# Kernel tuning notes

Measured on AMD Instinct MI355X. Metric: run time of the kernel, lower is better.

The kernel has to match this reference:

```python
import jax, jax.numpy as jnp
import numpy as np

B, T, C = 4, 2048, 1024
N_HEAD = 16
HEAD_DIM = C // N_HEAD


def setup_inputs() -> dict:
    key = jax.random.key(0)
    kx, kk, kq, kv, kp = jax.random.split(key, 5)
    s = 1.0 / np.sqrt(C)
    return {
        "x": jax.random.normal(kx, (B, T, C), dtype=jnp.float32),
        "Wk": jax.random.normal(kk, (C, C), dtype=jnp.float32) * s,
        "Wq": jax.random.normal(kq, (C, C), dtype=jnp.float32) * s,
        "Wv": jax.random.normal(kv, (C, C), dtype=jnp.float32) * s,
        "Wp": jax.random.normal(kp, (C, C), dtype=jnp.float32) * s,
    }


def reference(x, Wk, Wq, Wv, Wp):
    b, t, c = x.shape
    # torch nn.Linear(y = x @ W.T); split heads -> [B, H, T, D]
    def heads(w):
        return jnp.einsum("btc,ec->bte", x, w).reshape(b, t, N_HEAD, HEAD_DIM).transpose(0, 2, 1, 3)
    k = heads(Wk)
    q = heads(Wq)
    v = heads(Wv)
    scale = 1.0 / np.sqrt(HEAD_DIM).astype(np.float32)
    att = jnp.einsum("bhqd,bhkd->bhqk", q, k) * scale  # [B,H,T,T]
    causal = jnp.tril(jnp.ones((t, t), dtype=bool))
    att = jnp.where(causal[None, None], att, -jnp.inf)
    att = jax.nn.softmax(att, axis=-1)
    y = jnp.einsum("bhqk,bhkd->bhqd", att, v)  # [B,H,T,D]
    y = y.transpose(0, 2, 1, 3).reshape(b, t, c)
    return jnp.einsum("btc,ec->bte", y, Wp)
```

## Files before the change

### kernel.cpp

```cpp
#include <hip/hip_runtime.h>

typedef __bf16 bf16x8 __attribute__((ext_vector_type(8)));
typedef float f32x4 __attribute__((ext_vector_type(4)));
typedef float f32x16 __attribute__((ext_vector_type(16)));
typedef unsigned short u16x8 __attribute__((ext_vector_type(8)));
typedef unsigned short u16x4 __attribute__((ext_vector_type(4)));
typedef unsigned u32x4 __attribute__((ext_vector_type(4)));

#define BB 4
#define TT 2048
#define CC 1024
#define HH 16
#define DD 64

__device__ __forceinline__ unsigned short f2bf(float f){
  unsigned u = __builtin_bit_cast(unsigned, f);
  u += 0x7FFFu + ((u >> 16) & 1u);
  return (unsigned short)(u >> 16);
}
__device__ __forceinline__ bf16x8 as_bf(u16x8 v){ return __builtin_bit_cast(bf16x8, v); }
__device__ __forceinline__ unsigned cvt_pk(float lo, float hi){
  unsigned r; asm("v_cvt_pk_bf16_f32 %0, %1, %2" : "=v"(r) : "v"(lo), "v"(hi)); return r;
}
__device__ __forceinline__ void pl32swap(unsigned &a, unsigned &b){
  asm("v_permlane32_swap_b32 %0, %1" : "+v"(a), "+v"(b));
}
__device__ __forceinline__ float ex2(float x){
#if __has_builtin(__builtin_amdgcn_exp2f)
  return __builtin_amdgcn_exp2f(x);
#else
  return __expf(x * 0.6931471805599453f);
#endif
}

__global__ __launch_bounds__(256) void cvt_all(const float* __restrict__ x,
                                               const float* __restrict__ Wk,
                                               const float* __restrict__ Wq,
                                               const float* __restrict__ Wv,
                                               const float* __restrict__ Wp,
                                               unsigned short* __restrict__ xb,
                                               unsigned short* __restrict__ wb){
  const int i = blockIdx.x * 256 + threadIdx.x;
  constexpr int EX = (BB*TT*CC)/4;
  const float* src; unsigned short* dst; int off;
  if (i < EX){ src = x; dst = xb; off = i; }
  else {
    const int j = i - EX;
    const int wsel = j >> 18;
    off = j & 262143;
    src = (wsel==0) ? Wk : (wsel==1) ? Wq : (wsel==2) ? Wv : Wp;
    dst = wb + ((size_t)wsel << 20);
  }
  const float4 f = ((const float4*)src)[off];
  u16x4 o; o.x = f2bf(f.x); o.y = f2bf(f.y); o.z = f2bf(f.z); o.w = f2bf(f.w);
  ((u16x4*)dst)[off] = o;
}

template<int NX, bool QKV>
__global__ __launch_bounds__(256) void gemm128(const unsigned short* __restrict__ A,
                                               const unsigned short* __restrict__ Bm,
                                               void* __restrict__ o0, void* __restrict__ o1,
                                               void* __restrict__ o2){
  constexpr int K = 1024;
  constexpr int NWG = NX * 64;
  __shared__ __align__(16) unsigned short As[128*64];
  __shared__ __align__(16) unsigned short Bs[128*64];
  const int tid = threadIdx.x;
  const int flat = blockIdx.y * NX + blockIdx.x;
  const int swz = (flat & 7) * (NWG / 8) + (flat >> 3);
  const int n0 = (swz % NX) * 128;
  const int m0 = (swz / NX) * 128;
  const int w = tid >> 6, lane = tid & 63, l15 = lane & 15, g = lane >> 4;
  const int wm = (w >> 1) * 64, wn = (w & 1) * 64;
  const int tsel = QKV ? (n0 >> 10) : 0;

  f32x4 acc[4][4] = {};

  for (int k0 = 0; k0 < K; k0 += 64){
    #pragma unroll
    for (int i = 0; i < 4; ++i){
      const int p = i*256 + tid;
      const int r = p >> 3, c = p & 7;
      const int gc = c ^ (r & 7);
      __builtin_amdgcn_global_load_lds(
        (const __attribute__((address_space(1))) void*)(A + (size_t)(m0 + r)*K + k0 + gc*8),
        (__attribute__((address_space(3))) void*)(As + p*8), 16, 0, 0);
    }
    #pragma unroll
    for (int i = 0; i < 4; ++i){
      const int p = i*256 + tid;
      const int r = p >> 3, c = p & 7;
      const int gc = c ^ (r & 7);
      __builtin_amdgcn_global_load_lds(
        (const __attribute__((address_space(1))) void*)(Bm + (size_t)(n0 + r)*K + k0 + gc*8),
        (__attribute__((address_space(3))) void*)(Bs + p*8), 16, 0, 0);
    }
    __syncthreads();

    bf16x8 af[2][4], bfr[2][4];
    #pragma unroll
    for (int ks = 0; ks < 2; ++ks){
      #pragma unroll
      for (int m = 0; m < 4; ++m){
        const int R = wm + m*16 + l15;
        const int c = (ks*4 + g) ^ (R & 7);
        af[ks][m] = as_bf(*(const u16x8*)(As + R*64 + c*8));
      }
      #pragma unroll
      for (int n = 0; n < 4; ++n){
        const int R = wn + n*16 + l15;
        const int c = (ks*4 + g) ^ (R & 7);
        bfr[ks][n] = as_bf(*(const u16x8*)(Bs + R*64 + c*8));
      }
    }
    #pragma unroll
    for (int ks = 0; ks < 2; ++ks)
      #pragma unroll
      for (int m = 0; m < 4; ++m)
        #pragma unroll
        for (int n = 0; n < 4; ++n)
          acc[m][n] = __builtin_amdgcn_mfma_f32_16x16x32_bf16(af[ks][m], bfr[ks][n], acc[m][n], 0, 0, 0);
    __syncthreads();
  }

  if (QKV && tsel == 2){
    const int bq = m0 >> 11;
    const int t0 = m0 & 2047;
    unsigned short* vt = (unsigned short*)o2;
    #pragma unroll
    for (int n = 0; n < 4; ++n){
      const int cg = (n0 & 1023) + wn + n*16 + l15;
      const int h = cg >> 6, d = cg & 63;
      unsigned short* base = vt + ((size_t)(bq*HH + h)*DD + d)*TT;
      #pragma unroll
      for (int m = 0; m < 4; ++m){
        const int t = t0 + wm + m*16 + g*4;
        const int kt = t >> 6;
        const int cch = ((t >> 3) & 7) ^ (d & 7);
        u16x4 pv;
        pv.x = f2bf(acc[m][n][0]); pv.y = f2bf(acc[m][n][1]);
        pv.z = f2bf(acc[m][n][2]); pv.w = f2bf(acc[m][n][3]);
        *(u16x4*)(base + (size_t)kt*64 + cch*8 + (t & 7)) = pv;
      }
    }
    return;
  }

  const float sc = (QKV && tsel == 1) ? 0.18033688011112042f : 1.0f;
  unsigned short* outb = nullptr;
  if (QKV) outb = (unsigned short*)(tsel == 0 ? o0 : o1);

  #pragma unroll
  for (int m = 0; m < 4; ++m)
    #pragma unroll
    for (int n = 0; n < 4; ++n)
      #pragma unroll
      for (int r = 0; r < 4; ++r){
        const int row = m0 + wm + m*16 + g*4 + r;
        const int col = n0 + wn + n*16 + l15;
        const float v = acc[m][n][r];
        if (QKV) outb[(size_t)row*1024 + (col & 1023)] = f2bf(v * sc);
        else     ((float*)o0)[(size_t)row*1024 + col] = v;
      }
}

__global__ __launch_bounds__(512, 4) void attn2(const unsigned short* __restrict__ Q,
                                                const unsigned short* __restrict__ Km,
                                                const unsigned short* __restrict__ Vt,
                                                unsigned short* __restrict__ Y){
  __shared__ __align__(16) unsigned short Ks[3][64*64];
  __shared__ __align__(16) unsigned short Vs[3][64*64];
  const int bh = blockIdx.x, b = bh >> 4, h = bh & 15;
  const int yq = blockIdx.y;
  const int qt = (yq < 4) ? (7 - yq) : (yq - 4);
  const int tid = threadIdx.x;
  const int w = tid >> 6, lane = tid & 63, l31 = lane & 31, hi = lane >> 5;
  const int q0 = qt * 256;
  const int wq0 = q0 + w * 32;
  const int wqmax = wq0 + 31;
  const int nkt = 4 * qt + 4;
  const int qg = wq0 + l31;

  const unsigned short* Ksrc = Km + (size_t)b*TT*CC + h*DD;
  const unsigned short* Vsrc = Vt + (size_t)bh*DD*TT;

  auto stage = [&](int buf, int kt){
    const int r = tid >> 3, c = tid & 7;
    const int gc = c ^ (r & 7);
    __builtin_amdgcn_global_load_lds(
      (const __attribute__((address_space(1))) void*)(Ksrc + (size_t)(kt*64 + r)*CC + gc*8),
      (__attribute__((address_space(3))) void*)(&Ks[buf][tid*8]), 16, 0, 0);
    __builtin_amdgcn_global_load_lds(
      (const __attribute__((address_space(1))) void*)(Vsrc + (size_t)r*TT + (size_t)kt*64 + c*8),
      (__attribute__((address_space(3))) void*)(&Vs[buf][tid*8]), 16, 0, 0);
  };

  stage(0, 0);

  const unsigned short* qrow = Q + ((size_t)b*TT + wq0 + l31)*CC + h*DD;
  bf16x8 qf[4];
  #pragma unroll
  for (int ds = 0; ds < 4; ++ds)
    qf[ds] = as_bf(*(const u16x8*)(qrow + 16*ds + 8*hi));

  int koff[4];
  #pragma unroll
  for (int ds = 0; ds < 4; ++ds)
    koff[ds] = l31*64 + (((2*ds + hi) ^ (l31 & 7)) * 8);

  float m_ = -1e30f, l_ = 0.f;
  f32x16 y0 = {}, y1 = {};

  int cb = 0;
  for (int t = 0; t < nkt; ++t){
    const int nx = (cb == 2) ? 0 : cb + 1;
    if (t + 1 < nkt){
      stage(nx, t + 1);
      asm volatile("s_waitcnt vmcnt(2)" ::: "memory");
    } else {
      asm volatile("s_waitcnt vmcnt(0)" ::: "memory");
    }
    __builtin_amdgcn_s_barrier();

    if (t*64 <= wqmax){
      const unsigned short* Kp = &Ks[cb][0];
      const unsigned short* Vp = &Vs[cb][0];

      f32x16 s0 = {}, s1 = {};
      __builtin_amdgcn_s_setprio(1);
      #pragma unroll
      for (int ds = 0; ds < 4; ++ds){
        bf16x8 kf0 = as_bf(*(const u16x8*)(Kp + koff[ds]));
        s0 = __builtin_amdgcn_mfma_f32_32x32x16_bf16(kf0, qf[ds], s0, 0, 0, 0);
        bf16x8 kf1 = as_bf(*(const u16x8*)(Kp + koff[ds] + 2048));
        s1 = __builtin_amdgcn_mfma_f32_32x32x16_bf16(kf1, qf[ds], s1, 0, 0, 0);
      }
      __builtin_amdgcn_s_setprio(0);

      if (t*64 + 63 > wq0){
        const int kb0 = t*64;
        #pragma unroll
        for (int r = 0; r < 16; ++r){
          const int kr = (r & 3) + 8*(r >> 2) + 4*hi;
          if (kb0 + kr      > qg) s0[r] = -1e30f;
          if (kb0 + 32 + kr > qg) s1[r] = -1e30f;
        }
      }

      float tm[8];
      #pragma unroll
      for (int r = 0; r < 8; ++r) tm[r] = fmaxf(fmaxf(s0[r], s0[r+8]), fmaxf(s1[r], s1[r+8]));
      #pragma unroll
      for (int r = 0; r < 4; ++r) tm[r] = fmaxf(tm[r], tm[r+4]);
      float pmax = fmaxf(fmaxf(tm[0], tm[2]), fmaxf(tm[1], tm[3]));
      pmax = fmaxf(pmax, __shfl_xor(pmax, 32));

      if (!__all(pmax <= m_ + 8.f)){
        const float mnew = fmaxf(m_, pmax);
        const float alpha = ex2(m_ - mnew);
        l_ *= alpha;
        #pragma unroll
        for (int r = 0; r < 16; ++r){
          const float ar = __shfl(alpha, (r & 3) + 8*(r >> 2) + 4*hi);
          y0[r] *= ar; y1[r] *= ar;
        }
        m_ = mnew;
      }

      #pragma unroll
      for (int r = 0; r < 16; ++r) s0[r] = ex2(s0[r] - m_);
      #pragma unroll
      for (int r = 0; r < 16; ++r) s1[r] = ex2(s1[r] - m_);
      float ts[8];
      #pragma unroll
      for (int r = 0; r < 8; ++r) ts[r] = (s0[r] + s0[r+8]) + (s1[r] + s1[r+8]);
      #pragma unroll
      for (int r = 0; r < 4; ++r) ts[r] += ts[r+4];
      float rs = (ts[0] + ts[2]) + (ts[1] + ts[3]);
      rs += __shfl_xor(rs, 32);
      l_ += rs;

      __builtin_amdgcn_s_setprio(1);
      #pragma unroll
      for (int m = 0; m < 4; ++m){
        const f32x16 c = (m < 2) ? s0 : s1;
        const int bx = (m & 1) * 8;
        unsigned A0 = cvt_pk(c[bx+0], c[bx+1]);
        unsigned B0 = cvt_pk(c[bx+4], c[bx+5]);
        pl32swap(A0, B0);
        unsigned A1 = cvt_pk(c[bx+2], c[bx+3]);
        unsigned B1 = cvt_pk(c[bx+6], c[bx+7]);
        pl32swap(A1, B1);
        u32x4 pw; pw.x = A0; pw.y = A1; pw.z = B0; pw.w = B1;
        const bf16x8 pa = __builtin_bit_cast(bf16x8, pw);
        bf16x8 vf0 = as_bf(*(const u16x8*)(Vp + koff[m]));
        y0 = __builtin_amdgcn_mfma_f32_32x32x16_bf16(pa, vf0, y0, 0, 0, 0);
        bf16x8 vf1 = as_bf(*(const u16x8*)(Vp + koff[m] + 2048));
        y1 = __builtin_amdgcn_mfma_f32_32x32x16_bf16(pa, vf1, y1, 0, 0, 0);
      }
      __builtin_amdgcn_s_setprio(0);
    }
    cb = nx;
  }

  const float linv = 1.f / l_;
  #pragma unroll
  for (int r = 0; r < 16; ++r){
    const int qlr = (r & 3) + 8*(r >> 2) + 4*hi;
    const float lr = __shfl(linv, qlr);
    unsigned short* yp = Y + ((size_t)b*TT + wq0 + qlr)*CC + h*DD + l31;
    yp[0]  = f2bf(y0[r] * lr);
    yp[32] = f2bf(y1[r] * lr);
  }
}

extern "C" void kernel_launch(void* const* d_in, const int* in_sizes, int n_in,
                              void* d_out, int out_size, void* d_ws, size_t ws_size,
                              hipStream_t stream){
  const float* x  = (const float*)d_in[0];
  const float* Wk = (const float*)d_in[1];
  const float* Wq = (const float*)d_in[2];
  const float* Wv = (const float*)d_in[3];
  const float* Wp = (const float*)d_in[4];

  const size_t E  = (size_t)BB*TT*CC;
  const size_t Wn = (size_t)CC*CC;
  unsigned short* ws  = (unsigned short*)d_ws;
  unsigned short* xb  = ws;
  unsigned short* wkb = xb  + E;
  unsigned short* wqb = wkb + Wn;
  unsigned short* wvb = wqb + Wn;
  unsigned short* wpb = wvb + Wn;
  unsigned short* qb  = wpb + Wn;
  unsigned short* kb  = qb  + E;
  unsigned short* vt  = kb  + E;

  cvt_all<<<12288, 256, 0, stream>>>(x, Wk, Wq, Wv, Wp, xb, wkb);

  gemm128<24, true><<<dim3(24, 64), 256, 0, stream>>>(xb, wkb, kb, qb, vt);

  unsigned short* yb = xb;
  attn2<<<dim3(BB*HH, TT/256), 512, 0, stream>>>(qb, kb, vt, yb);

  gemm128<8, false><<<dim3(8, 64), 256, 0, stream>>>(yb, wpb, (float*)d_out, nullptr, nullptr);
}
```

Baseline: 159.4 us.

## Use 256x256 double-buffered QKV GEMM with async LDS prefetch

Replaces the 128x128 single-buffered QKV projection GEMM with a 256x256-tile, 512-thread kernel. It uses 128KB of dynamic LDS for two stages, so the next K-tile's global-to-LDS loads are in flight while the current tile runs on MFMA, and it raises MFMA priority around the inner loop. The larger tile is meant to improve operand reuse and hide global latency. In exchange the grid shrinks to 384 workgroups with one per CU, which risks poor tail balance on a 256-CU part and higher register pressure from the 8x4 accumulator array.

```diff
diff --git a/kernel.cpp b/kernel.cpp
--- a/kernel.cpp
+++ b/kernel.cpp
@@ -56,11 +56,132 @@
   ((u16x4*)dst)[off] = o;
 }
 
-template<int NX, bool QKV>
+template<int NX>
+__global__ __launch_bounds__(512) void gemm256q(const unsigned short* __restrict__ A,
+                                                const unsigned short* __restrict__ Bm,
+                                                void* __restrict__ o0, void* __restrict__ o1,
+                                                void* __restrict__ o2){
+  constexpr int K = 1024;
+  constexpr int NKT = 16;
+  constexpr int NWG = NX * 32;
+  extern __shared__ unsigned short lds[];
+  const int tid = threadIdx.x;
+  const int flat = blockIdx.y * NX + blockIdx.x;
+  const int swz = (flat & 7) * (NWG / 8) + (flat >> 3);
+  const int n0 = (swz % NX) * 256;
+  const int m0 = (swz / NX) * 256;
+  const int w = tid >> 6, lane = tid & 63, l15 = lane & 15, g = lane >> 4;
+  const int wm = (w >> 2) * 128;
+  const int wn = (w & 3) * 64;
+  const int tsel = n0 >> 10;
+
+  auto stage = [&](int s, int kt){
+    unsigned short* Asl = lds + s*32768;
+    unsigned short* Bsl = Asl + 16384;
+    const int k0 = kt * 64;
+    #pragma unroll
+    for (int i = 0; i < 4; ++i){
+      const int p = i*512 + tid;
+      const int r = p >> 3, c = p & 7;
+      const int gc = c ^ (r & 7);
+      __builtin_amdgcn_global_load_lds(
+        (const __attribute__((address_space(1))) void*)(A + (size_t)(m0 + r)*K + k0 + gc*8),
+        (__attribute__((address_space(3))) void*)(Asl + p*8), 16, 0, 0);
+    }
+    #pragma unroll
+    for (int i = 0; i < 4; ++i){
+      const int p = i*512 + tid;
+      const int r = p >> 3, c = p & 7;
+      const int gc = c ^ (r & 7);
+      __builtin_amdgcn_global_load_lds(
+        (const __attribute__((address_space(1))) void*)(Bm + (size_t)(n0 + r)*K + k0 + gc*8),
+        (__attribute__((address_space(3))) void*)(Bsl + p*8), 16, 0, 0);
+    }
+  };
+
+  f32x4 acc[8][4] = {};
+  stage(0, 0);
+
+  for (int t = 0; t < NKT; ++t){
+    const int s = t & 1;
+    if (t + 1 < NKT){
+      stage(s ^ 1, t + 1);
+      asm volatile("s_waitcnt vmcnt(8)" ::: "memory");
+    } else {
+      asm volatile("s_waitcnt vmcnt(0)" ::: "memory");
+    }
+    __builtin_amdgcn_s_barrier();
+
+    const unsigned short* Asl = lds + s*32768;
+    const unsigned short* Bsl = Asl + 16384;
+
+    #pragma unroll
+    for (int ks = 0; ks < 2; ++ks){
+      bf16x8 b4[4];
+      #pragma unroll
+      for (int n = 0; n < 4; ++n){
+        const int R = wn + n*16 + l15;
+        const int c = (ks*4 + g) ^ (R & 7);
+        b4[n] = as_bf(*(const u16x8*)(Bsl + R*64 + c*8));
+      }
+      __builtin_amdgcn_s_setprio(1);
+      #pragma unroll
+      for (int m = 0; m < 8; ++m){
+        const int R = wm + m*16 + l15;
+        const int c = (ks*4 + g) ^ (R & 7);
+        bf16x8 a = as_bf(*(const u16x8*)(Asl + R*64 + c*8));
+        #pragma unroll
+        for (int n = 0; n < 4; ++n)
+          acc[m][n] = __builtin_amdgcn_mfma_f32_16x16x32_bf16(a, b4[n], acc[m][n], 0, 0, 0);
+      }
+      __builtin_amdgcn_s_setprio(0);
+    }
+
+    asm volatile("s_waitcnt lgkmcnt(0)" ::: "memory");
+    __builtin_amdgcn_s_barrier();
+  }
+
+  if (tsel == 2){
+    const int bq = m0 >> 11;
+    const int t0 = m0 & 2047;
+    unsigned short* vt = (unsigned short*)o2;
+    #pragma unroll
+    for (int n = 0; n < 4; ++n){
+      const int cg = (n0 & 1023) + wn + n*16 + l15;
+      const int h = cg >> 6, d = cg & 63;
+      unsigned short* base = vt + ((size_t)(bq*HH + h)*DD + d)*TT;
+      #pragma unroll
+      for (int m = 0; m < 8; ++m){
+        const int t = t0 + wm + m*16 + g*4;
+        const int kt = t >> 6;
+        const int cch = ((t >> 3) & 7) ^ (d & 7);
+        u16x4 pv;
+        pv.x = f2bf(acc[m][n][0]); pv.y = f2bf(acc[m][n][1]);
+        pv.z = f2bf(acc[m][n][2]); pv.w = f2bf(acc[m][n][3]);
+        *(u16x4*)(base + (size_t)kt*64 + cch*8 + (t & 7)) = pv;
+      }
+    }
+    return;
+  }
+
+  const float sc = (tsel == 1) ? 0.18033688011112042f : 1.0f;
+  unsigned short* outb = (unsigned short*)(tsel == 0 ? o0 : o1);
+  #pragma unroll
+  for (int m = 0; m < 8; ++m)
+    #pragma unroll
+    for (int n = 0; n < 4; ++n)
+      #pragma unroll
+      for (int r = 0; r < 4; ++r){
+        const int row = m0 + wm + m*16 + g*4 + r;
+        const int col = (n0 & 1023) + wn + n*16 + l15;
+        outb[(size_t)row*1024 + col] = f2bf(acc[m][n][r] * sc);
+      }
+}
+
+template<int NX>
 __global__ __launch_bounds__(256) void gemm128(const unsigned short* __restrict__ A,
                                                const unsigned short* __restrict__ Bm,
-                                               void* __restrict__ o0, void* __restrict__ o1,
-                                               void* __restrict__ o2){
+                                               float* __restrict__ o0){
   constexpr int K = 1024;
   constexpr int NWG = NX * 64;
   __shared__ __align__(16) unsigned short As[128*64];
@@ -72,7 +193,6 @@
   const int m0 = (swz / NX) * 128;
   const int w = tid >> 6, lane = tid & 63, l15 = lane & 15, g = lane >> 4;
   const int wm = (w >> 1) * 64, wn = (w & 1) * 64;
-  const int tsel = QKV ? (n0 >> 10) : 0;
 
   f32x4 acc[4][4] = {};
 
@@ -123,33 +243,6 @@
     __syncthreads();
   }
 
-  if (QKV && tsel == 2){
-    const int bq = m0 >> 11;
-    const int t0 = m0 & 2047;
-    unsigned short* vt = (unsigned short*)o2;
-    #pragma unroll
-    for (int n = 0; n < 4; ++n){
-      const int cg = (n0 & 1023) + wn + n*16 + l15;
-      const int h = cg >> 6, d = cg & 63;
-      unsigned short* base = vt + ((size_t)(bq*HH + h)*DD + d)*TT;
-      #pragma unroll
-      for (int m = 0; m < 4; ++m){
-        const int t = t0 + wm + m*16 + g*4;
-        const int kt = t >> 6;
-        const int cch = ((t >> 3) & 7) ^ (d & 7);
-        u16x4 pv;
-        pv.x = f2bf(acc[m][n][0]); pv.y = f2bf(acc[m][n][1]);
-        pv.z = f2bf(acc[m][n][2]); pv.w = f2bf(acc[m][n][3]);
-        *(u16x4*)(base + (size_t)kt*64 + cch*8 + (t & 7)) = pv;
-      }
-    }
-    return;
-  }
-
-  const float sc = (QKV && tsel == 1) ? 0.18033688011112042f : 1.0f;
-  unsigned short* outb = nullptr;
-  if (QKV) outb = (unsigned short*)(tsel == 0 ? o0 : o1);
-
   #pragma unroll
   for (int m = 0; m < 4; ++m)
     #pragma unroll
@@ -158,9 +251,7 @@
       for (int r = 0; r < 4; ++r){
         const int row = m0 + wm + m*16 + g*4 + r;
         const int col = n0 + wn + n*16 + l15;
-        const float v = acc[m][n][r];
-        if (QKV) outb[(size_t)row*1024 + (col & 1023)] = f2bf(v * sc);
-        else     ((float*)o0)[(size_t)row*1024 + col] = v;
+        o0[(size_t)row*1024 + col] = acc[m][n][r];
       }
 }
 
@@ -335,12 +426,17 @@
   unsigned short* kb  = qb  + E;
   unsigned short* vt  = kb  + E;
 
+  (void)wqb; (void)wvb;
+
+  hipFuncSetAttribute(reinterpret_cast<const void*>(gemm256q<12>),
+                      hipFuncAttributeMaxDynamicSharedMemorySize, 131072);
+
   cvt_all<<<12288, 256, 0, stream>>>(x, Wk, Wq, Wv, Wp, xb, wkb);
 
-  gemm128<24, true><<<dim3(24, 64), 256, 0, stream>>>(xb, wkb, kb, qb, vt);
+  gemm256q<12><<<dim3(12, 32), 512, 131072, stream>>>(xb, wkb, kb, qb, vt);
 
   unsigned short* yb = xb;
   attn2<<<dim3(BB*HH, TT/256), 512, 0, stream>>>(qb, kb, vt, yb);
 
-  gemm128<8, false><<<dim3(8, 64), 256, 0, stream>>>(yb, wpb, (float*)d_out, nullptr, nullptr);
-}
+  gemm128<8><<<dim3(8, 64), 256, 0, stream>>>(yb, wpb, (float*)d_out);
+}
```

New measurement: 158.7 us. Within noise of the previous version (-0.4%).

## Use dedicated 256x128 QKV GEMM with 32x32x16 MFMA tiles

Applied to the files above, without the earlier changes.

Moves the fused QKV projection into its own kernel with 256x128 block tiles, so each wave computes a 128x64 sub-tile using 32x32x16 bf16 MFMAs instead of 16x16x32. The aim is more reuse of the A and B fragments loaded from LDS per MFMA, and half as many workgroups each reloading the weight tile. It also raises MFMA issue priority around the inner loop and sets launch bounds to allow two blocks per CU. The trade-off is larger accumulator register use (128 floats per thread) and more LDS per block, which may limit occupancy; the output projection GEMM is simplified to fp32-only output.

```diff
diff --git a/kernel.cpp b/kernel.cpp
--- a/kernel.cpp
+++ b/kernel.cpp
@@ -56,11 +56,112 @@
   ((u16x4*)dst)[off] = o;
 }
 
-template<int NX, bool QKV>
+__global__ __launch_bounds__(256, 2) void gemmqkv(const unsigned short* __restrict__ A,
+                                                  const unsigned short* __restrict__ Bm,
+                                                  void* __restrict__ o0, void* __restrict__ o1,
+                                                  void* __restrict__ o2){
+  constexpr int K = 1024;
+  __shared__ __align__(16) unsigned short As[256*64];
+  __shared__ __align__(16) unsigned short Bs[128*64];
+  const int tid = threadIdx.x;
+  const int flat = blockIdx.y * 24 + blockIdx.x;
+  const int swz = (flat & 7) * 96 + (flat >> 3);
+  const int n0 = (swz % 24) * 128;
+  const int m0 = (swz / 24) * 256;
+  const int w = tid >> 6, lane = tid & 63, l31 = lane & 31, hi = lane >> 5;
+  const int wm = (w >> 1) * 128, wn = (w & 1) * 64;
+  const int tsel = n0 >> 10;
+
+  f32x16 acc[4][2] = {};
+
+  for (int k0 = 0; k0 < K; k0 += 64){
+    #pragma unroll
+    for (int i = 0; i < 8; ++i){
+      const int p = i*256 + tid;
+      const int r = p >> 3, c = p & 7;
+      const int gc = c ^ (r & 7);
+      __builtin_amdgcn_global_load_lds(
+        (const __attribute__((address_space(1))) void*)(A + (size_t)(m0 + r)*K + k0 + gc*8),
+        (__attribute__((address_space(3))) void*)(As + p*8), 16, 0, 0);
+    }
+    #pragma unroll
+    for (int i = 0; i < 4; ++i){
+      const int p = i*256 + tid;
+      const int r = p >> 3, c = p & 7;
+      const int gc = c ^ (r & 7);
+      __builtin_amdgcn_global_load_lds(
+        (const __attribute__((address_space(1))) void*)(Bm + (size_t)(n0 + r)*K + k0 + gc*8),
+        (__attribute__((address_space(3))) void*)(Bs + p*8), 16, 0, 0);
+    }
+    __syncthreads();
+
+    #pragma unroll
+    for (int ks = 0; ks < 4; ++ks){
+      bf16x8 bf2[2];
+      #pragma unroll
+      for (int nb = 0; nb < 2; ++nb){
+        const int R = wn + nb*32 + l31;
+        const int cc = (2*ks + hi) ^ (R & 7);
+        bf2[nb] = as_bf(*(const u16x8*)(Bs + R*64 + cc*8));
+      }
+      __builtin_amdgcn_s_setprio(1);
+      #pragma unroll
+      for (int mb = 0; mb < 4; ++mb){
+        const int R = wm + mb*32 + l31;
+        const int cc = (2*ks + hi) ^ (R & 7);
+        bf16x8 a = as_bf(*(const u16x8*)(As + R*64 + cc*8));
+        acc[mb][0] = __builtin_amdgcn_mfma_f32_32x32x16_bf16(a, bf2[0], acc[mb][0], 0, 0, 0);
+        acc[mb][1] = __builtin_amdgcn_mfma_f32_32x32x16_bf16(a, bf2[1], acc[mb][1], 0, 0, 0);
+      }
+      __builtin_amdgcn_s_setprio(0);
+    }
+    __syncthreads();
+  }
+
+  if (tsel == 2){
+    const int bq = m0 >> 11;
+    const int t0b = m0 & 2047;
+    unsigned short* vt = (unsigned short*)o2;
+    #pragma unroll
+    for (int nb = 0; nb < 2; ++nb){
+      const int cg = (n0 & 1023) + wn + nb*32 + l31;
+      const int h = cg >> 6, d = cg & 63;
+      unsigned short* base = vt + ((size_t)(bq*HH + h)*DD + d)*TT;
+      #pragma unroll
+      for (int mb = 0; mb < 4; ++mb)
+        #pragma unroll
+        for (int q = 0; q < 4; ++q){
+          const int t = t0b + wm + mb*32 + 8*q + 4*hi;
+          const int kt = t >> 6;
+          const int cch = ((t >> 3) & 7) ^ (d & 7);
+          u16x4 pv;
+          pv.x = f2bf(acc[mb][nb][4*q+0]); pv.y = f2bf(acc[mb][nb][4*q+1]);
+          pv.z = f2bf(acc[mb][nb][4*q+2]); pv.w = f2bf(acc[mb][nb][4*q+3]);
+          *(u16x4*)(base + (size_t)kt*64 + cch*8 + (t & 7)) = pv;
+        }
+    }
+    return;
+  }
+
+  const float sc = (tsel == 1) ? 0.18033688011112042f : 1.0f;
+  unsigned short* outb = (unsigned short*)(tsel == 0 ? o0 : o1);
+  #pragma unroll
+  for (int mb = 0; mb < 4; ++mb)
+    #pragma unroll
+    for (int nb = 0; nb < 2; ++nb){
+      const int col = (n0 & 1023) + wn + nb*32 + l31;
+      #pragma unroll
+      for (int r = 0; r < 16; ++r){
+        const int row = m0 + wm + mb*32 + (r & 3) + 8*(r >> 2) + 4*hi;
+        outb[(size_t)row*1024 + col] = f2bf(acc[mb][nb][r] * sc);
+      }
+    }
+}
+
+template<int NX>
 __global__ __launch_bounds__(256) void gemm128(const unsigned short* __restrict__ A,
                                                const unsigned short* __restrict__ Bm,
-                                               void* __restrict__ o0, void* __restrict__ o1,
-                                               void* __restrict__ o2){
+                                               float* __restrict__ o0){
   constexpr int K = 1024;
   constexpr int NWG = NX * 64;
   __shared__ __align__(16) unsigned short As[128*64];
@@ -72,7 +173,6 @@
   const int m0 = (swz / NX) * 128;
   const int w = tid >> 6, lane = tid & 63, l15 = lane & 15, g = lane >> 4;
   const int wm = (w >> 1) * 64, wn = (w & 1) * 64;
-  const int tsel = QKV ? (n0 >> 10) : 0;
 
   f32x4 acc[4][4] = {};
 
@@ -123,33 +223,6 @@
     __syncthreads();
   }
 
-  if (QKV && tsel == 2){
-    const int bq = m0 >> 11;
-    const int t0 = m0 & 2047;
-    unsigned short* vt = (unsigned short*)o2;
-    #pragma unroll
-    for (int n = 0; n < 4; ++n){
-      const int cg = (n0 & 1023) + wn + n*16 + l15;
-      const int h = cg >> 6, d = cg & 63;
-      unsigned short* base = vt + ((size_t)(bq*HH + h)*DD + d)*TT;
-      #pragma unroll
-      for (int m = 0; m < 4; ++m){
-        const int t = t0 + wm + m*16 + g*4;
-        const int kt = t >> 6;
-        const int cch = ((t >> 3) & 7) ^ (d & 7);
-        u16x4 pv;
-        pv.x = f2bf(acc[m][n][0]); pv.y = f2bf(acc[m][n][1]);
-        pv.z = f2bf(acc[m][n][2]); pv.w = f2bf(acc[m][n][3]);
-        *(u16x4*)(base + (size_t)kt*64 + cch*8 + (t & 7)) = pv;
-      }
-    }
-    return;
-  }
-
-  const float sc = (QKV && tsel == 1) ? 0.18033688011112042f : 1.0f;
-  unsigned short* outb = nullptr;
-  if (QKV) outb = (unsigned short*)(tsel == 0 ? o0 : o1);
-
   #pragma unroll
   for (int m = 0; m < 4; ++m)
     #pragma unroll
@@ -158,9 +231,7 @@
       for (int r = 0; r < 4; ++r){
         const int row = m0 + wm + m*16 + g*4 + r;
         const int col = n0 + wn + n*16 + l15;
-        const float v = acc[m][n][r];
-        if (QKV) outb[(size_t)row*1024 + (col & 1023)] = f2bf(v * sc);
-        else     ((float*)o0)[(size_t)row*1024 + col] = v;
+        o0[(size_t)row*1024 + col] = acc[m][n][r];
       }
 }
 
@@ -335,12 +406,14 @@
   unsigned short* kb  = qb  + E;
   unsigned short* vt  = kb  + E;
 
+  (void)wqb; (void)wvb;
+
   cvt_all<<<12288, 256, 0, stream>>>(x, Wk, Wq, Wv, Wp, xb, wkb);
 
-  gemm128<24, true><<<dim3(24, 64), 256, 0, stream>>>(xb, wkb, kb, qb, vt);
+  gemmqkv<<<dim3(24, 32), 256, 0, stream>>>(xb, wkb, kb, qb, vt);
 
   unsigned short* yb = xb;
   attn2<<<dim3(BB*HH, TT/256), 512, 0, stream>>>(qb, kb, vt, yb);
 
-  gemm128<8, false><<<dim3(8, 64), 256, 0, stream>>>(yb, wpb, (float*)d_out, nullptr, nullptr);
-}
+  gemm128<8><<<dim3(8, 64), 256, 0, stream>>>(yb, wpb, (float*)d_out);
+}
```

New measurement: 164.9 us. 3.5% more time.
